# Kernel tuning notes

Hardware: AMD Instinct MI355X
Metric: run time of the kernel (lower is better)

The kernel has to match this reference:

```python
import jax, jax.numpy as jnp
import numpy as np

NEG_INF = -1e9
HIDDEN = 1024
HEADS = 16
SPH = HIDDEN // HEADS  # 64
B, Q, M = 8, 512, 512
R = Q + M


def rel_shift(x):
    # x: [N, H, Q, R] -> TransformerXL relative shift
    N, H, Qd, Rd = x.shape
    x = jnp.pad(x, ((0, 0), (0, 0), (0, 0), (1, 0)))
    x = x.reshape(N, H, Rd + 1, Qd)
    return x[:, :, 1:, :].reshape(N, H, Qd, Rd)


def setup_inputs() -> dict:
    key = jax.random.key(0)
    ks = jax.random.split(key, 11)
    std = 1.0 / np.sqrt(HIDDEN)
    # causal token mask: query position i (global pos M+i) may attend to ref pos j <= M+i
    q_pos = jnp.arange(Q)[:, None] + M
    r_pos = jnp.arange(R)[None, :]
    token_mask = (r_pos > q_pos).astype(jnp.float32)[None, None]  # [1,1,Q,R]
    return {
        "query_seqs": jax.random.normal(ks[0], (B, Q, HIDDEN), jnp.float32),
        "memory_seqs": jax.random.normal(ks[1], (B, M, HIDDEN), jnp.float32),
        "positional_encoding": jax.random.normal(ks[2], (R, HIDDEN), jnp.float32),
        "token_mask": token_mask,
        "content_bias": jax.random.normal(ks[3], (HEADS, SPH), jnp.float32) * 0.02,
        "position_bias": jax.random.normal(ks[4], (HEADS, SPH), jnp.float32) * 0.02,
        "Wq": jax.random.normal(ks[5], (HIDDEN, HEADS, SPH), jnp.float32) * std,
        "Wkc": jax.random.normal(ks[6], (HIDDEN, HEADS, SPH), jnp.float32) * std,
        "Wkp": jax.random.normal(ks[7], (HIDDEN, HEADS, SPH), jnp.float32) * std,
        "Wv": jax.random.normal(ks[8], (HIDDEN, HEADS, SPH), jnp.float32) * std,
        "Wo": jax.random.normal(ks[9], (HEADS, SPH, HIDDEN), jnp.float32) * std,
    }


def reference(query_seqs, memory_seqs, positional_encoding, token_mask,
              content_bias, position_bias, Wq, Wkc, Wkp, Wv, Wo):
    reference_seqs = jnp.concatenate([memory_seqs, query_seqs], axis=1)  # [B,R,D]
    query = jnp.einsum('nqd,dhs->nqhs', query_seqs, Wq)            # [B,Q,H,S]
    key_content = jnp.einsum('nrd,dhs->nrhs', reference_seqs, Wkc)  # [B,R,H,S]
    key_position = jnp.einsum('rd,dhs->rhs', positional_encoding, Wkp)  # [R,H,S]
    value = jnp.einsum('nrd,dhs->nrhs', reference_seqs, Wv)         # [B,R,H,S]

    content = jnp.einsum('nqhs,nrhs->nhqr', query + content_bias, key_content)
    positions = jnp.einsum('nqhs,rhs->nhqr', query + position_bias, key_position)
    positions = rel_shift(positions)

    scores = (content + positions) / np.sqrt(SPH) + token_mask * NEG_INF
    attn = jax.nn.softmax(scores, axis=3)  # [B,H,Q,R]
    out = jnp.einsum('nhqr,nrhs->nqhs', attn, value)
    return jnp.einsum('nqhs,hsd->nqd', out, Wo)  # [B,Q,D]
```

## Files before the change

kernel.cpp:

```cpp
#include <hip/hip_runtime.h>

#define B_ 8
#define Q_ 512
#define M_ 512
#define R_ 1024
#define H_ 16
#define S_ 64
#define D_ 1024
#define MEG 1048576L

typedef unsigned short ushort_t;
typedef __attribute__((ext_vector_type(8))) _Float16 f16x8;
typedef __attribute__((ext_vector_type(8))) unsigned short u16x8;
typedef __attribute__((ext_vector_type(4))) unsigned short u16x4;
typedef __attribute__((ext_vector_type(4))) float f32x4;
typedef __attribute__((ext_vector_type(2))) unsigned int u32x2;

__device__ __forceinline__ unsigned short h2u(_Float16 h) {
    union { _Float16 h; unsigned short u; } v; v.h = h; return v.u;
}
__device__ __forceinline__ unsigned int pk_f16(float a, float b) {
    union { _Float16 h[2]; unsigned int u; } v;
    v.h[0] = (_Float16)a; v.h[1] = (_Float16)b; return v.u;
}
__device__ __forceinline__ void async_cp16(const ushort_t* g, ushort_t* l) {
    __builtin_amdgcn_global_load_lds(
        (const __attribute__((address_space(1))) void*)g,
        (__attribute__((address_space(3))) void*)l, 16, 0, 0);
}

__global__ __launch_bounds__(256) void zero_out_f32_k(float* __restrict__ p, int n) {
    int i = blockIdx.x * 256 + threadIdx.x;
    if (i < n) p[i] = 0.f;
}

__global__ __launch_bounds__(256) void prep_k(
    const float* __restrict__ mem, const float* __restrict__ qry,
    const float* __restrict__ pos, const float* __restrict__ cb,
    const float* __restrict__ pb,
    const float* __restrict__ Wkc, const float* __restrict__ Wv,
    const float* __restrict__ Wkp, const float* __restrict__ Wq,
    const float* __restrict__ Wo,
    ushort_t* __restrict__ qcat, ushort_t* __restrict__ posb,
    ushort_t* __restrict__ cbpb, ushort_t* __restrict__ BT4,
    ushort_t* __restrict__ WoT) {
    int x = blockIdx.x, y = blockIdx.y, t = threadIdx.x;
    if (y < 5) {
        const float* in; ushort_t* out;
        switch (y) {
            case 0: in = Wkc; out = BT4;           break;
            case 1: in = Wv;  out = BT4 + MEG;     break;
            case 2: in = Wkp; out = BT4 + 2 * MEG; break;
            case 3: in = Wq;  out = BT4 + 3 * MEG; break;
            default: in = Wo; out = WoT;           break;
        }
        __shared__ ushort_t tile[32][33];
        int bx = (x & 31) * 32, by = (x >> 5) * 32;
        int tx = t & 31, ty = t >> 5;
        #pragma unroll
        for (int i = 0; i < 32; i += 8)
            tile[ty + i][tx] = h2u((_Float16)in[(long)(by + ty + i) * 1024 + bx + tx]);
        __syncthreads();
        #pragma unroll
        for (int i = 0; i < 32; i += 8)
            out[(long)(bx + ty + i) * 1024 + by + tx] = tile[tx][ty + i];
    } else if (y < 13) {
        int g = y - 5, r = x;
        const float* src = (r < 512) ? (mem + ((long)g * 512 + r) * 1024)
                                     : (qry + ((long)g * 512 + (r - 512)) * 1024);
        ushort_t* dst = qcat + ((long)g * 1024 + r) * 1024;
        int i = t * 4;
        f32x4 v = *(const f32x4*)(src + i);
        u32x2 o; o[0] = pk_f16(v[0], v[1]); o[1] = pk_f16(v[2], v[3]);
        *(u32x2*)(dst + i) = o;
    } else if (y == 13) {
        int i = t * 4;
        f32x4 v = *(const f32x4*)(pos + (long)x * 1024 + i);
        u32x2 o; o[0] = pk_f16(v[0], v[1]); o[1] = pk_f16(v[2], v[3]);
        *(u32x2*)(posb + (long)x * 1024 + i) = o;
    } else {
        if (x == 0) {
            for (int i = t; i < 1024; i += 256) {
                cbpb[i]        = h2u((_Float16)cb[i]);
                cbpb[1024 + i] = h2u((_Float16)pb[i]);
            }
        }
    }
}

__device__ __forceinline__ void gemm_body(const ushort_t* Arow0,
                                          const ushort_t* BTrow0,
                                          void* Crow0, long crs, int mode) {
    __shared__ __align__(16) ushort_t Al[3][128 * 32];
    __shared__ __align__(16) ushort_t Bl[3][128 * 32];

    int t = threadIdx.x;
    int wave = t >> 6, lane = t & 63, quad = lane >> 4, l16 = lane & 15;
    int wm = (wave & 1) * 64, wn = (wave >> 1) * 64;

    f32x4 acc[4][4];
    #pragma unroll
    for (int im = 0; im < 4; ++im)
        #pragma unroll
        for (int in = 0; in < 4; ++in) acc[im][in] = (f32x4){0.f, 0.f, 0.f, 0.f};

    int grow = lane >> 2, gcol = (lane & 3) * 8;
    const ushort_t* ga0 = Arow0 + (long)(wave * 32 + grow) * 1024 + gcol;
    const ushort_t* ga1 = Arow0 + (long)(wave * 32 + 16 + grow) * 1024 + gcol;
    const ushort_t* gb0 = BTrow0 + (long)(wave * 32 + grow) * 1024 + gcol;
    const ushort_t* gb1 = BTrow0 + (long)(wave * 32 + 16 + grow) * 1024 + gcol;
    int lo0 = (wave * 2 + 0) * 512;
    int lo1 = (wave * 2 + 1) * 512;

    #define STAGE_(buf, kst) do {                          \
        int k0_ = (kst) * 32;                              \
        async_cp16(ga0 + k0_, &Al[buf][lo0]);              \
        async_cp16(ga1 + k0_, &Al[buf][lo1]);              \
        async_cp16(gb0 + k0_, &Bl[buf][lo0]);              \
        async_cp16(gb1 + k0_, &Bl[buf][lo1]);              \
    } while (0)

    STAGE_(0, 0);
    STAGE_(1, 1);

    for (int j = 0; j < 32; ++j) {
        if (j < 31) asm volatile("s_waitcnt vmcnt(4)" ::: "memory");
        else        asm volatile("s_waitcnt vmcnt(0)" ::: "memory");
        __builtin_amdgcn_s_barrier();
        if (j + 2 < 32) STAGE_((j + 2) % 3, j + 2);

        int cb = j % 3;
        f16x8 af[4], bf[4];
        #pragma unroll
        for (int im = 0; im < 4; ++im)
            af[im] = *(const f16x8*)&Al[cb][(wm + im * 16 + l16) * 32 + quad * 8];
        #pragma unroll
        for (int in = 0; in < 4; ++in)
            bf[in] = *(const f16x8*)&Bl[cb][(wn + in * 16 + l16) * 32 + quad * 8];
        __builtin_amdgcn_s_setprio(1);
        #pragma unroll
        for (int im = 0; im < 4; ++im)
            #pragma unroll
            for (int in = 0; in < 4; ++in)
                acc[im][in] = __builtin_amdgcn_mfma_f32_16x16x32_f16(
                    af[im], bf[in], acc[im][in], 0, 0, 0);
        __builtin_amdgcn_s_setprio(0);
    }
    #undef STAGE_

    if (mode == 2) {
        #pragma unroll
        for (int im = 0; im < 4; ++im)
            #pragma unroll
            for (int in = 0; in < 4; ++in) {
                u16x4 pk;
                #pragma unroll
                for (int reg = 0; reg < 4; ++reg) pk[reg] = h2u((_Float16)acc[im][in][reg]);
                long addr = (long)(wn + in * 16 + l16) * 1024 + wm + im * 16 + quad * 4;
                *(u16x4*)((ushort_t*)Crow0 + addr) = pk;
            }
        return;
    }
    #pragma unroll
    for (int im = 0; im < 4; ++im)
        #pragma unroll
        for (int in = 0; in < 4; ++in)
            #pragma unroll
            for (int reg = 0; reg < 4; ++reg) {
                long addr = (long)(wm + im * 16 + quad * 4 + reg) * crs
                          + wn + in * 16 + l16;
                if (mode == 1) ((float*)Crow0)[addr] = acc[im][in][reg];
                else ((ushort_t*)Crow0)[addr] = h2u((_Float16)acc[im][in][reg]);
            }
}

__global__ __launch_bounds__(256) void gemm_mega(
    const ushort_t* __restrict__ qcat, const ushort_t* __restrict__ posb,
    const ushort_t* __restrict__ BT4,
    ushort_t* __restrict__ kcC, ushort_t* __restrict__ vT,
    ushort_t* __restrict__ qproj, ushort_t* __restrict__ kpp) {
    int id = blockIdx.x;
    if (id < 1024) {
        int z = id >> 7, tl = id & 127;
        int x = tl >> 4, y = tl & 15;
        const ushort_t* Arow0 = qcat + (long)z * MEG + (long)x * 128 * 1024;
        if (y < 8) {
            gemm_body(Arow0, BT4 + (long)y * 128 * 1024,
                      kcC + (long)z * MEG + (long)x * 128 * 1024 + y * 128, 1024, 0);
        } else {
            int n0 = (y - 8) * 128;
            gemm_body(Arow0, BT4 + (long)(1024 + n0) * 1024,
                      vT + ((long)z * 1024 + n0) * 1024 + x * 128, 0, 2);
        }
    } else if (id < 1088) {
        int u = id - 1024;
        int x = u >> 3, y = u & 7;
        gemm_body(posb + (long)x * 128 * 1024,
                  BT4 + (long)(2048 + y * 128) * 1024,
                  kpp + (long)x * 128 * 1024 + y * 128, 1024, 0);
    } else {
        int u = id - 1088;
        int b = u >> 5, v2 = u & 31;
        int x = v2 >> 3, y = v2 & 7;
        gemm_body(qcat + (long)b * MEG + (long)(512 + x * 128) * 1024,
                  BT4 + (long)(3072 + y * 128) * 1024,
                  qproj + (long)b * 512 * 1024 + (long)x * 128 * 1024 + y * 128, 1024, 0);
    }
}

__global__ __launch_bounds__(256) void gemm_fin(
    const ushort_t* __restrict__ A, const ushort_t* __restrict__ WoT,
    float* __restrict__ out) {
    gemm_body(A + (long)blockIdx.x * 128 * 1024,
              WoT + (long)blockIdx.y * 128 * 1024,
              out + (long)blockIdx.x * 128 * 1024 + blockIdx.y * 128, 1024, 1);
}

__global__ __launch_bounds__(512) void attn_kernel(
    const ushort_t* __restrict__ qproj,
    const ushort_t* __restrict__ kc,
    const ushort_t* __restrict__ kp,
    const ushort_t* __restrict__ vT,
    const ushort_t* __restrict__ cbpb,
    ushort_t* __restrict__ aout)
{
    int qt = (blockIdx.x + ((blockIdx.y >> 6) << 1)) & 3;
    int q0 = qt * 128;
    int bh = blockIdx.y;
    int b = bh >> 4, h = bh & 15;
    int t = threadIdx.x;
    int wave = t >> 6, lane = t & 63, quad = lane >> 4, l16 = lane & 15;

    __shared__ __align__(16) ushort_t Kc[64][72];
    __shared__ __align__(16) ushort_t Vt[64][72];
    __shared__ __align__(16) ushort_t Kp[192][72];
    __shared__ __align__(16) char Pu[8][2304];
    ushort_t* Pl = (ushort_t*)&Pu[wave][0];

    const ushort_t* qrow = qproj + ((long)(b * Q_ + q0 + wave * 16 + l16)) * 1024 + h * 64;
    f16x8 qcf[2], qpf[2];
    #pragma unroll
    for (int ks = 0; ks < 2; ++ks) {
        f16x8 qv  = *(const f16x8*)(qrow + ks * 32 + quad * 8);
        f16x8 cbv = *(const f16x8*)(cbpb + h * 64 + ks * 32 + quad * 8);
        f16x8 pbv = *(const f16x8*)(cbpb + 1024 + h * 64 + ks * 32 + quad * 8);
        qcf[ks] = qv + cbv;
        qpf[ks] = qv + pbv;
    }

    float m_s[4];
    f32x4 o_acc[4], ls4;
    #pragma unroll
    for (int r = 0; r < 4; ++r) {
        m_s[r] = -1e30f;
        o_acc[r] = (f32x4){0.f, 0.f, 0.f, 0.f};
    }
    ls4 = (f32x4){0.f, 0.f, 0.f, 0.f};

    f16x8 ones;
    #pragma unroll
    for (int j = 0; j < 8; ++j) ones[j] = (_Float16)1.0f;

    int srow = t >> 3, sc0 = (t & 7) * 8;
    const ushort_t* kcb = kc + ((long)(b * R_) + srow) * 1024 + h * 64 + sc0;
    const ushort_t* vtb = vT + ((long)(b * 1024 + h * 64 + srow)) * 1024 + sc0;
    const ushort_t* kpb = kp + h * 64 + sc0;

    int ntiles = ((q0 + 639) >> 6) + 1;

    u16x8 rKc = *(const u16x8*)(kcb);
    u16x8 rVt = *(const u16x8*)(vtb);
    u16x8 rKp[3];
    {
        int jb0 = 384 - q0;
        #pragma unroll
        for (int p = 0; p < 3; ++p) {
            int j = jb0 + p * 64 + srow;
            int jc = j > 1023 ? 1023 : j;
            rKp[p] = *(const u16x8*)(kpb + (long)jc * 1024);
        }
    }

    for (int it = 0; it < ntiles; ++it) {
        int r0 = it * 64;
        int jbase = r0 - q0 + 384;
        int gb0 = jbase >> 4;
        __syncthreads();
        *(u16x8*)&Kc[srow][sc0] = rKc;
        *(u16x8*)&Vt[srow][sc0] = rVt;
        if (it == 0) {
            #pragma unroll
            for (int p = 0; p < 3; ++p) {
                int j = jbase + p * 64 + srow;
                int ph = ((j >> 4) % 12) * 16 + (j & 15);
                *(u16x8*)&Kp[ph][sc0] = rKp[p];
            }
        } else {
            int j = jbase + 128 + srow;
            int ph = ((j >> 4) % 12) * 16 + (j & 15);
            *(u16x8*)&Kp[ph][sc0] = rKp[0];
        }
        __syncthreads();
        if (it + 1 < ntiles) {
            int r1 = r0 + 64;
            rKc = *(const u16x8*)(kcb + (long)r1 * 1024);
            rVt = *(const u16x8*)(vtb + r1);
            int j = r1 - q0 + 512 + srow;
            int jc = j > 1023 ? 1023 : j;
            rKp[0] = *(const u16x8*)(kpb + (long)jc * 1024);
        }

        f32x4 sc[4];
        #pragma unroll
        for (int s = 0; s < 4; ++s) sc[s] = (f32x4){0.f, 0.f, 0.f, 0.f};
        f32x4 dd[5];
        #pragma unroll
        for (int s = 0; s < 5; ++s) dd[s] = (f32x4){0.f, 0.f, 0.f, 0.f};

        __builtin_amdgcn_s_setprio(1);
        #pragma unroll
        for (int ks = 0; ks < 2; ++ks)
            #pragma unroll
            for (int sub = 0; sub < 4; ++sub) {
                f16x8 bb = *(const f16x8*)&Kc[sub * 16 + l16][ks * 32 + quad * 8];
                sc[sub] = __builtin_amdgcn_mfma_f32_16x16x32_f16(qcf[ks], bb, sc[sub], 0, 0, 0);
            }
        #pragma unroll
        for (int ks = 0; ks < 2; ++ks)
            #pragma unroll
            for (int sub = 0; sub < 5; ++sub) {
                int pb = (gb0 + 7 - wave + sub) % 12;
                f16x8 bb = *(const f16x8*)&Kp[pb * 16 + l16][ks * 32 + quad * 8];
                dd[sub] = __builtin_amdgcn_mfma_f32_16x16x32_f16(qpf[ks], bb, dd[sub], 0, 0, 0);
            }
        __builtin_amdgcn_s_setprio(0);

        #pragma unroll
        for (int reg = 0; reg < 4; ++reg) {
            int row16 = quad * 4 + reg;
            int src = (lane & 48) + ((l16 + 15 - row16) & 15);
            float dsh[5];
            #pragma unroll
            for (int sub = 0; sub < 5; ++sub)
                dsh[sub] = __shfl(dd[sub][reg], src);
            #pragma unroll
            for (int sub = 0; sub < 4; ++sub) {
                float dval = (l16 > row16) ? dsh[sub + 1] : dsh[sub];
                float sv = (sc[sub][reg] + dval) * 0.125f;
                int rl = sub * 16 + l16;
                if (r0 + rl > q0 + wave * 16 + row16 + 512) sv = -1e30f;
                sc[sub][reg] = sv;
            }
        }

        float vmax[4];
        #pragma unroll
        for (int reg = 0; reg < 4; ++reg)
            vmax[reg] = fmaxf(fmaxf(sc[0][reg], sc[1][reg]),
                              fmaxf(sc[2][reg], sc[3][reg]));
        int ok = (vmax[0] <= m_s[0] + 8.f) & (vmax[1] <= m_s[1] + 8.f) &
                 (vmax[2] <= m_s[2] + 8.f) & (vmax[3] <= m_s[3] + 8.f);
        if (!__all(ok)) {
            #pragma unroll
            for (int reg = 0; reg < 4; ++reg) {
                float rm = vmax[reg];
                #pragma unroll
                for (int m = 1; m < 16; m <<= 1) rm = fmaxf(rm, __shfl_xor(rm, m));
                float mn = fmaxf(m_s[reg], rm);
                float alpha = __expf(m_s[reg] - mn);
                m_s[reg] = mn;
                ls4[reg] *= alpha;
                #pragma unroll
                for (int sub = 0; sub < 4; ++sub)
                    o_acc[sub][reg] *= alpha;
            }
        }
        #pragma unroll
        for (int sub = 0; sub < 4; ++sub)
            #pragma unroll
            for (int reg = 0; reg < 4; ++reg) {
                float p = __expf(sc[sub][reg] - m_s[reg]);
                Pl[(quad * 4 + reg) * 72 + sub * 16 + l16] = h2u((_Float16)p);
            }

        f16x8 a0 = *(const f16x8*)&Pl[l16 * 72 + quad * 8];
        f16x8 a1 = *(const f16x8*)&Pl[l16 * 72 + 32 + quad * 8];
        __builtin_amdgcn_s_setprio(1);
        ls4 = __builtin_amdgcn_mfma_f32_16x16x32_f16(a0, ones, ls4, 0, 0, 0);
        ls4 = __builtin_amdgcn_mfma_f32_16x16x32_f16(a1, ones, ls4, 0, 0, 0);
        #pragma unroll
        for (int sub = 0; sub < 4; ++sub) {
            f16x8 bb0 = *(const f16x8*)&Vt[sub * 16 + l16][quad * 8];
            o_acc[sub] = __builtin_amdgcn_mfma_f32_16x16x32_f16(a0, bb0, o_acc[sub], 0, 0, 0);
            f16x8 bb1 = *(const f16x8*)&Vt[sub * 16 + l16][32 + quad * 8];
            o_acc[sub] = __builtin_amdgcn_mfma_f32_16x16x32_f16(a1, bb1, o_acc[sub], 0, 0, 0);
        }
        __builtin_amdgcn_s_setprio(0);
    }

    #pragma unroll
    for (int reg = 0; reg < 4; ++reg) {
        float inv = 1.f / ls4[reg];
        int qg = q0 + wave * 16 + quad * 4 + reg;
        ushort_t* orow = aout + ((long)(b * Q_ + qg)) * 1024 + h * 64;
        #pragma unroll
        for (int sub = 0; sub < 4; ++sub)
            orow[sub * 16 + l16] = h2u((_Float16)(o_acc[sub][reg] * inv));
    }
}

extern "C" void kernel_launch(void* const* d_in, const int* in_sizes, int n_in,
                              void* d_out, int out_size, void* d_ws, size_t ws_size,
                              hipStream_t stream) {
    const float* query  = (const float*)d_in[0];
    const float* memory = (const float*)d_in[1];
    const float* pos    = (const float*)d_in[2];
    const float* cb  = (const float*)d_in[4];
    const float* pb  = (const float*)d_in[5];
    const float* Wq  = (const float*)d_in[6];
    const float* Wkc = (const float*)d_in[7];
    const float* Wkp = (const float*)d_in[8];
    const float* Wv  = (const float*)d_in[9];
    const float* Wo  = (const float*)d_in[10];
    float* out = (float*)d_out;
    ushort_t* ws = (ushort_t*)d_ws;

    size_t ws_elems = ws_size / 2;
    if (ws_elems < 36 * MEG) {
        zero_out_f32_k<<<(out_size + 255) / 256, 256, 0, stream>>>(out, out_size);
        return;
    }

    ushort_t* cbpb  = ws;
    ushort_t* BT4   = ws + MEG;
    ushort_t* WoT   = BT4 + 4 * MEG;
    ushort_t* kpp   = WoT + MEG;
    ushort_t* posb  = kpp + MEG;
    ushort_t* qproj = posb + MEG;
    ushort_t* kcC   = qproj + 4 * MEG;
    ushort_t* vT    = kcC + 8 * MEG;
    ushort_t* qcat  = vT + 8 * MEG;
    ushort_t* aout  = qproj;

    prep_k<<<dim3(1024, 15), 256, 0, stream>>>(
        memory, query, pos, cb, pb, Wkc, Wv, Wkp, Wq, Wo,
        qcat, posb, cbpb, BT4, WoT);
    gemm_mega<<<dim3(1344), 256, 0, stream>>>(qcat, posb, BT4, kcC, vT, qproj, kpp);
    attn_kernel<<<dim3(4, 128), 512, 0, stream>>>(qproj, kcC, kpp, vT, cbpb, aout);
    gemm_fin<<<dim3(32, 8, 1), 256, 0, stream>>>(aout, WoT, out);
}
```

Measured before the change: 252.9 us.

## Restructure projection GEMM to 512 threads, BK=64, swizzled LDS, 4-stage ring

Rewrites the shared GEMM body used by the projection and output kernels. Blocks grow from 4 to 8 waves, each computing a 64x32 sub-tile. The K step doubles to 64 with a 4-buffer LDS ring that prefetches two stages ahead. LDS rows get an XOR swizzle to avoid bank conflicts, and async copies are interleaved with MFMA sub-steps. This aims to raise latency hiding and cut barrier count, but uses 128KB of LDS per block, which limits occupancy to one block per CU.

```diff
diff --git a/kernel.cpp b/kernel.cpp
--- a/kernel.cpp
+++ b/kernel.cpp
@@ -91,90 +91,104 @@
 __device__ __forceinline__ void gemm_body(const ushort_t* Arow0,
                                           const ushort_t* BTrow0,
                                           void* Crow0, long crs, int mode) {
-    __shared__ __align__(16) ushort_t Al[3][128 * 32];
-    __shared__ __align__(16) ushort_t Bl[3][128 * 32];
+    __shared__ __align__(16) ushort_t Al[4][128 * 64];
+    __shared__ __align__(16) ushort_t Bl[4][128 * 64];
 
     int t = threadIdx.x;
     int wave = t >> 6, lane = t & 63, quad = lane >> 4, l16 = lane & 15;
-    int wm = (wave & 1) * 64, wn = (wave >> 1) * 64;
-
-    f32x4 acc[4][4];
-    #pragma unroll
-    for (int im = 0; im < 4; ++im)
-        #pragma unroll
-        for (int in = 0; in < 4; ++in) acc[im][in] = (f32x4){0.f, 0.f, 0.f, 0.f};
-
-    int grow = lane >> 2, gcol = (lane & 3) * 8;
-    const ushort_t* ga0 = Arow0 + (long)(wave * 32 + grow) * 1024 + gcol;
-    const ushort_t* ga1 = Arow0 + (long)(wave * 32 + 16 + grow) * 1024 + gcol;
-    const ushort_t* gb0 = BTrow0 + (long)(wave * 32 + grow) * 1024 + gcol;
-    const ushort_t* gb1 = BTrow0 + (long)(wave * 32 + 16 + grow) * 1024 + gcol;
-    int lo0 = (wave * 2 + 0) * 512;
-    int lo1 = (wave * 2 + 1) * 512;
-
-    #define STAGE_(buf, kst) do {                          \
-        int k0_ = (kst) * 32;                              \
-        async_cp16(ga0 + k0_, &Al[buf][lo0]);              \
-        async_cp16(ga1 + k0_, &Al[buf][lo1]);              \
-        async_cp16(gb0 + k0_, &Bl[buf][lo0]);              \
-        async_cp16(gb1 + k0_, &Bl[buf][lo1]);              \
-    } while (0)
-
-    STAGE_(0, 0);
-    STAGE_(1, 1);
-
-    for (int j = 0; j < 32; ++j) {
-        if (j < 31) asm volatile("s_waitcnt vmcnt(4)" ::: "memory");
-        else        asm volatile("s_waitcnt vmcnt(0)" ::: "memory");
+    int wm = (wave & 1) * 64;
+    int wn = (wave >> 1) * 32;
+
+    f32x4 acc[4][2];
+    #pragma unroll
+    for (int f = 0; f < 4; ++f)
+        #pragma unroll
+        for (int g = 0; g < 2; ++g) acc[f][g] = (f32x4){0.f, 0.f, 0.f, 0.f};
+
+    int grow = t >> 3;
+    int gcol = ((t & 7) * 8) ^ (((t >> 5) & 1) * 16) ^ (((t >> 6) & 1) * 32);
+    const ushort_t* ga[2] = { Arow0 + (long)grow * 1024 + gcol,
+                              Arow0 + (long)(64 + grow) * 1024 + gcol };
+    const ushort_t* gb[2] = { BTrow0 + (long)grow * 1024 + gcol,
+                              BTrow0 + (long)(64 + grow) * 1024 + gcol };
+    int ldst = wave * 512;
+
+    #pragma unroll
+    for (int i = 0; i < 2; ++i) {
+        async_cp16(ga[i], &Al[0][i * 4096 + ldst]);
+        async_cp16(gb[i], &Bl[0][i * 4096 + ldst]);
+    }
+    #pragma unroll
+    for (int i = 0; i < 2; ++i) {
+        async_cp16(ga[i] + 64, &Al[1][i * 4096 + ldst]);
+        async_cp16(gb[i] + 64, &Bl[1][i * 4096 + ldst]);
+    }
+
+    int rswz = (l16 & 12) << 2;
+
+    #pragma unroll
+    for (int kt = 0; kt < 16; ++kt) {
+        if (kt < 15) asm volatile("s_waitcnt vmcnt(4)" ::: "memory");
+        else         asm volatile("s_waitcnt vmcnt(0)" ::: "memory");
         __builtin_amdgcn_s_barrier();
-        if (j + 2 < 32) STAGE_((j + 2) % 3, j + 2);
-
-        int cb = j % 3;
-        f16x8 af[4], bf[4];
-        #pragma unroll
-        for (int im = 0; im < 4; ++im)
-            af[im] = *(const f16x8*)&Al[cb][(wm + im * 16 + l16) * 32 + quad * 8];
-        #pragma unroll
-        for (int in = 0; in < 4; ++in)
-            bf[in] = *(const f16x8*)&Bl[cb][(wn + in * 16 + l16) * 32 + quad * 8];
-        __builtin_amdgcn_s_setprio(1);
-        #pragma unroll
-        for (int im = 0; im < 4; ++im)
-            #pragma unroll
-            for (int in = 0; in < 4; ++in)
-                acc[im][in] = __builtin_amdgcn_mfma_f32_16x16x32_f16(
-                    af[im], bf[in], acc[im][in], 0, 0, 0);
-        __builtin_amdgcn_s_setprio(0);
-    }
-    #undef STAGE_
+        const int cb = kt & 3, nb = (kt + 2) & 3;
+
+        #pragma unroll
+        for (int p = 0; p < 4; ++p) {
+            if (kt + 2 < 16) {
+                if (p < 2) async_cp16(ga[p] + (kt + 2) * 64, &Al[nb][p * 4096 + ldst]);
+                else       async_cp16(gb[p - 2] + (kt + 2) * 64, &Bl[nb][(p - 2) * 4096 + ldst]);
+            }
+            const int mh = p & 1, nh = p >> 1;
+            f16x8 af[2][2], bf[2];
+            #pragma unroll
+            for (int f = 0; f < 2; ++f)
+                #pragma unroll
+                for (int ks = 0; ks < 2; ++ks)
+                    af[f][ks] = *(const f16x8*)&Al[cb][(wm + (mh * 2 + f) * 16 + l16) * 64
+                                                       + ((ks * 32 + quad * 8) ^ rswz)];
+            #pragma unroll
+            for (int ks = 0; ks < 2; ++ks)
+                bf[ks] = *(const f16x8*)&Bl[cb][(wn + nh * 16 + l16) * 64
+                                                + ((ks * 32 + quad * 8) ^ rswz)];
+            __builtin_amdgcn_s_setprio(1);
+            #pragma unroll
+            for (int f = 0; f < 2; ++f)
+                #pragma unroll
+                for (int ks = 0; ks < 2; ++ks)
+                    acc[mh * 2 + f][nh] = __builtin_amdgcn_mfma_f32_16x16x32_f16(
+                        af[f][ks], bf[ks], acc[mh * 2 + f][nh], 0, 0, 0);
+            __builtin_amdgcn_s_setprio(0);
+        }
+    }
 
     if (mode == 2) {
         #pragma unroll
-        for (int im = 0; im < 4; ++im)
-            #pragma unroll
-            for (int in = 0; in < 4; ++in) {
+        for (int f = 0; f < 4; ++f)
+            #pragma unroll
+            for (int g = 0; g < 2; ++g) {
                 u16x4 pk;
                 #pragma unroll
-                for (int reg = 0; reg < 4; ++reg) pk[reg] = h2u((_Float16)acc[im][in][reg]);
-                long addr = (long)(wn + in * 16 + l16) * 1024 + wm + im * 16 + quad * 4;
+                for (int reg = 0; reg < 4; ++reg) pk[reg] = h2u((_Float16)acc[f][g][reg]);
+                long addr = (long)(wn + g * 16 + l16) * 1024 + wm + f * 16 + quad * 4;
                 *(u16x4*)((ushort_t*)Crow0 + addr) = pk;
             }
         return;
     }
     #pragma unroll
-    for (int im = 0; im < 4; ++im)
-        #pragma unroll
-        for (int in = 0; in < 4; ++in)
+    for (int f = 0; f < 4; ++f)
+        #pragma unroll
+        for (int g = 0; g < 2; ++g)
             #pragma unroll
             for (int reg = 0; reg < 4; ++reg) {
-                long addr = (long)(wm + im * 16 + quad * 4 + reg) * crs
-                          + wn + in * 16 + l16;
-                if (mode == 1) ((float*)Crow0)[addr] = acc[im][in][reg];
-                else ((ushort_t*)Crow0)[addr] = h2u((_Float16)acc[im][in][reg]);
-            }
-}
-
-__global__ __launch_bounds__(256) void gemm_mega(
+                long addr = (long)(wm + f * 16 + quad * 4 + reg) * crs
+                          + wn + g * 16 + l16;
+                if (mode == 1) ((float*)Crow0)[addr] = acc[f][g][reg];
+                else ((ushort_t*)Crow0)[addr] = h2u((_Float16)acc[f][g][reg]);
+            }
+}
+
+__global__ __launch_bounds__(512) void gemm_mega(
     const ushort_t* __restrict__ qcat, const ushort_t* __restrict__ posb,
     const ushort_t* __restrict__ BT4,
     ushort_t* __restrict__ kcC, ushort_t* __restrict__ vT,
@@ -208,7 +222,7 @@
     }
 }
 
-__global__ __launch_bounds__(256) void gemm_fin(
+__global__ __launch_bounds__(512) void gemm_fin(
     const ushort_t* __restrict__ A, const ushort_t* __restrict__ WoT,
     float* __restrict__ out) {
     gemm_body(A + (long)blockIdx.x * 128 * 1024,
@@ -445,7 +459,7 @@
     prep_k<<<dim3(1024, 15), 256, 0, stream>>>(
         memory, query, pos, cb, pb, Wkc, Wv, Wkp, Wq, Wo,
         qcat, posb, cbpb, BT4, WoT);
-    gemm_mega<<<dim3(1344), 256, 0, stream>>>(qcat, posb, BT4, kcC, vT, qproj, kpp);
+    gemm_mega<<<dim3(1344), 512, 0, stream>>>(qcat, posb, BT4, kcC, vT, qproj, kpp);
     attn_kernel<<<dim3(4, 128), 512, 0, stream>>>(qproj, kcC, kpp, vT, cbpb, aout);
-    gemm_fin<<<dim3(32, 8, 1), 256, 0, stream>>>(aout, WoT, out);
-}
+    gemm_fin<<<dim3(32, 8, 1), 512, 0, stream>>>(aout, WoT, out);
+}
```

Measured after the change: 284.1 us. +12.3%, slower.
